# Kernel tuning notes

Hardware: AMD Instinct MI355X
Metric: run time of the kernel (lower is better)

Reference implementation:

```python
import jax, jax.numpy as jnp
import numpy as np

BN_EPS = 1e-5
R = 8.0        # radius
L = 11         # sequence kernel size (odd), s = L//2
K = 24         # kernel_channels[-1]
N_NODES = 32768
N_EDGES = 524288
C_IN = 128     # in_channels == out_channels
C_W = 32       # width = out_channels * base_width / 64


def _bn(x, gamma, beta):
    # BatchNorm1d in training mode: biased batch statistics over node dim
    mu = jnp.mean(x, axis=0)
    var = jnp.mean(jnp.square(x - mu), axis=0)
    return (x - mu) * jax.lax.rsqrt(var + BN_EPS) * gamma + beta


def _lrelu(x, slope):
    return jnp.where(x >= 0, x, slope * x)


def setup_inputs() -> dict:
    key = jax.random.key(0)
    ks = jax.random.split(key, 10)

    def glorot(k, shape, fan_in):
        return jax.random.normal(k, shape, jnp.float32) * np.float32(1.0 / np.sqrt(fan_in))

    inp = {}
    inp["x"] = jax.random.normal(ks[0], (N_NODES, C_IN), jnp.float32)
    inp["pos"] = jax.random.normal(ks[1], (N_NODES, 3), jnp.float32) * 10.0
    inp["ori"] = jax.random.normal(ks[2], (N_NODES, 9), jnp.float32)
    inp["seq"] = jnp.arange(N_NODES, dtype=jnp.int32)
    inp["edge_index"] = jax.random.randint(ks[3], (2, N_EDGES), 0, N_NODES, jnp.int32)
    # input MLP params: BN(C_IN) -> LeakyReLU(0.1) -> Linear(C_IN->C_W, no bias) -> BN(C_W) -> LeakyReLU(0.1)
    inp["bn1_g"] = jnp.ones((C_IN,), jnp.float32)
    inp["bn1_b"] = jnp.zeros((C_IN,), jnp.float32)
    inp["lin1_w"] = glorot(ks[4], (C_IN, C_W), C_IN)
    inp["bn2_g"] = jnp.ones((C_W,), jnp.float32)
    inp["bn2_b"] = jnp.zeros((C_W,), jnp.float32)
    # CDConv WeightNet (single layer kernel_channels=[K]): per-seq-bin affine 7 -> K
    inp["wn_w"] = glorot(ks[5], (L, 7, K), 7)
    inp["wn_b"] = jnp.zeros((L, K), jnp.float32)
    # CDConv output projection: [K*C_W, C_W]
    inp["conv_w"] = glorot(ks[6], (K * C_W, C_W), K * C_W)
    # output Linear: BN(C_W) -> LeakyReLU(0.1) -> Linear(C_W->C_IN, no bias)
    inp["bn3_g"] = jnp.ones((C_W,), jnp.float32)
    inp["bn3_b"] = jnp.zeros((C_W,), jnp.float32)
    inp["lin2_w"] = glorot(ks[7], (C_W, C_IN), C_W)
    return inp


def reference(x, pos, ori, seq, edge_index,
              bn1_g, bn1_b, lin1_w, bn2_g, bn2_b,
              wn_w, wn_b, conv_w, bn3_g, bn3_b, lin2_w):
    n = x.shape[0]
    identity = x  # in_channels == out_channels -> identity branch is passthrough

    # ----- input MLP (mid_channels=None) -----
    h = _lrelu(_bn(x, bn1_g, bn1_b), 0.1)
    h = h @ lin1_w                       # [N, C_W]
    h = _lrelu(_bn(h, bn2_g, bn2_b), 0.1)

    # ----- CDConv: continuous geometric kernel over neighbor edges -----
    src, dst = edge_index[0], edge_index[1]      # message j=src -> i=dst
    d = pos[src] - pos[dst]                      # [E,3]
    dist = jnp.linalg.norm(d, axis=-1, keepdims=True)
    direction = d / (dist + 1e-9)
    Ri = ori[dst].reshape(-1, 3, 3)              # receiver local frame
    Rj = ori[src].reshape(-1, 3, 3)
    pos_local = jnp.einsum('eij,ej->ei', Ri, direction)      # direction in local frame
    ori_feat = jnp.einsum('eij,ej->ei', Ri, Rj[:, 0, :])     # neighbor axis in local frame
    delta = jnp.concatenate([pos_local, ori_feat, dist / R], axis=-1)  # [E,7]

    s = L // 2
    sidx = jnp.clip(seq[src] - seq[dst], -s, s) + s          # [E] in [0, L)

    # WeightNet: per-edge affine selected by sequence bin, LeakyReLU(0.2)
    w = _lrelu(jnp.einsum('ef,efk->ek', delta, wn_w[sidx]) + wn_b[sidx], 0.2)  # [E,K]

    # message = outer(kernel_weight, x_j), scatter-sum to receivers
    msg = (w[:, :, None] * h[src][:, None, :]).reshape(w.shape[0], K * C_W)   # [E, K*C_W]
    agg = jax.ops.segment_sum(msg, dst, num_segments=n)                        # [N, K*C_W]
    h = agg @ conv_w                                                            # [N, C_W]

    # ----- output Linear + residual -----
    h = _lrelu(_bn(h, bn3_g, bn3_b), 0.1)
    out = h @ lin2_w + identity
    return out
```

## Files before the change

kernel.cpp:

```cpp
#include <hip/hip_runtime.h>

#define N_NODES 32768
#define C_IN 128
#define C_W 32
#define KK 24
#define SS 5
#define NPB 8
#define TC 256
#define AGS (KK * C_W + 4)
#define WNS 172
#define WBS 28
#define HS 36

#define BF_LO(u) __uint_as_float((u) << 16)
#define BF_HI(u) __uint_as_float((u) & 0xFFFF0000u)

__device__ __forceinline__ unsigned int bf16pair(float lo, float hi) {
    unsigned int ulo = __float_as_uint(lo);
    unsigned int uhi = __float_as_uint(hi);
    ulo = (ulo + 0x7FFFu + ((ulo >> 16) & 1u)) >> 16;
    uhi = (uhi + 0x7FFFu + ((uhi >> 16) & 1u)) & 0xFFFF0000u;
    return uhi | ulo;
}

__global__ void __launch_bounds__(256) k_pre(
        const float* __restrict__ x, float* __restrict__ s1,
        const int* __restrict__ ei, int E, int* __restrict__ counts) {
    int t = threadIdx.x;
    int c = t % C_IN;
    int r0 = blockIdx.x * 2 + t / C_IN;
    float s = 0.f, sq = 0.f;
    for (int r = r0; r < N_NODES; r += 1024) {
        float v = x[(size_t)r * C_IN + c];
        s += v; sq += v * v;
    }
    atomicAdd(&s1[c], s);
    atomicAdd(&s1[C_IN + c], sq);
    for (int e = blockIdx.x * 256 + t; e < E; e += 512 * 256)
        atomicAdd(&counts[ei[E + e]], 1);
}

__global__ void __launch_bounds__(256) k_mlp1(
        const float* __restrict__ x, const float* __restrict__ s1,
        const float* __restrict__ g1, const float* __restrict__ b1,
        const float* __restrict__ w1, float* __restrict__ hpre,
        float* __restrict__ s2sh) {
    __shared__ float sAB[2][C_IN];
    __shared__ float sx[32][C_IN + 4];
    __shared__ float sw[C_IN][C_W];
    const int t = threadIdx.x;
    const int row0 = blockIdx.x * 32;
    if (t < C_IN) {
        float mean = s1[t] * (1.f / N_NODES);
        float var = s1[C_IN + t] * (1.f / N_NODES) - mean * mean;
        float a = g1[t] * rsqrtf(var + 1e-5f);
        sAB[0][t] = a; sAB[1][t] = b1[t] - mean * a;
    }
    for (int idx = t; idx < C_IN * C_W; idx += 256)
        sw[idx / C_W][idx % C_W] = w1[idx];
    __syncthreads();
    for (int idx = t; idx < 32 * 32; idx += 256) {
        int r = idx >> 5, cq = idx & 31;
        float4 v = *(const float4*)&x[(size_t)(row0 + r) * C_IN + cq * 4];
        float* d = &sx[r][cq * 4];
        float a0 = sAB[0][cq*4+0]*v.x + sAB[1][cq*4+0];
        float a1 = sAB[0][cq*4+1]*v.y + sAB[1][cq*4+1];
        float a2 = sAB[0][cq*4+2]*v.z + sAB[1][cq*4+2];
        float a3 = sAB[0][cq*4+3]*v.w + sAB[1][cq*4+3];
        d[0] = a0 >= 0.f ? a0 : 0.1f * a0;
        d[1] = a1 >= 0.f ? a1 : 0.1f * a1;
        d[2] = a2 >= 0.f ? a2 : 0.1f * a2;
        d[3] = a3 >= 0.f ? a3 : 0.1f * a3;
    }
    __syncthreads();
    const int r = t >> 3, c0 = (t & 7) * 4;
    float ac0 = 0.f, ac1 = 0.f, ac2 = 0.f, ac3 = 0.f;
    #pragma unroll 8
    for (int cc = 0; cc < C_IN; ++cc) {
        float xv = sx[r][cc];
        float4 wv = *(const float4*)&sw[cc][c0];
        ac0 += xv * wv.x; ac1 += xv * wv.y; ac2 += xv * wv.z; ac3 += xv * wv.w;
    }
    float4 o; o.x = ac0; o.y = ac1; o.z = ac2; o.w = ac3;
    *(float4*)&hpre[(size_t)(row0 + r) * C_W + c0] = o;
    __syncthreads();
    sx[r][c0] = ac0; sx[r][c0+1] = ac1; sx[r][c0+2] = ac2; sx[r][c0+3] = ac3;
    __syncthreads();
    if (t < C_W) {
        float s = 0.f, sq = 0.f;
        #pragma unroll
        for (int rr = 0; rr < 32; ++rr) {
            float v = sx[rr][t];
            s += v; sq += v * v;
        }
        int sh = (blockIdx.x & 7) * 64;
        atomicAdd(&s2sh[sh + t], s);
        atomicAdd(&s2sh[sh + C_W + t], sq);
    }
}

__global__ void __launch_bounds__(1024) k_scan(
        const int* __restrict__ counts, int* __restrict__ offsets,
        int* __restrict__ cursor) {
    __shared__ int sblk[1024];
    const int t = threadIdx.x;
    const int base = t * 32;
    const int4* cp = (const int4*)(counts + base);
    int loc[32];
    int s = 0;
    #pragma unroll
    for (int q = 0; q < 8; ++q) {
        int4 v = cp[q];
        loc[q*4+0] = s; s += v.x;
        loc[q*4+1] = s; s += v.y;
        loc[q*4+2] = s; s += v.z;
        loc[q*4+3] = s; s += v.w;
    }
    sblk[t] = s;
    __syncthreads();
    for (int d = 1; d < 1024; d <<= 1) {
        int u = (t >= d) ? sblk[t - d] : 0;
        __syncthreads();
        sblk[t] += u;
        __syncthreads();
    }
    const int blockbase = sblk[t] - s;
    #pragma unroll
    for (int q = 0; q < 8; ++q) {
        int4 o;
        o.x = blockbase + loc[q*4+0];
        o.y = blockbase + loc[q*4+1];
        o.z = blockbase + loc[q*4+2];
        o.w = blockbase + loc[q*4+3];
        ((int4*)(offsets + base))[q] = o;
        ((int4*)(cursor + base))[q] = o;
    }
    if (t == 1023) offsets[N_NODES] = sblk[1023];
}

__global__ void __launch_bounds__(256) k_scatter(
        const int* __restrict__ ei, int E, int* __restrict__ cursor,
        int* __restrict__ srcPerm) {
    int e = blockIdx.x * 256 + threadIdx.x;
    if (e < E) {
        int dst = ei[E + e];
        int p = atomicAdd(&cursor[dst], 1);
        srcPerm[p] = ei[e];
    }
}

__global__ void __launch_bounds__(512) k_mega(
    const int* __restrict__ offsets, const int* __restrict__ srcPerm,
    const float* __restrict__ pos, const float* __restrict__ ori,
    const int* __restrict__ seq, const float* __restrict__ hpre,
    const float* __restrict__ s2sh, const float* __restrict__ g2,
    const float* __restrict__ b2,
    const float* __restrict__ wnw, const float* __restrict__ wnb,
    const float* __restrict__ convw,
    float* __restrict__ convout, float* __restrict__ s3sh) {

    __shared__ float sWnw[11 * WNS];
    __shared__ float sWnb[11 * WBS];
    __shared__ float sA2[C_W], sB2[C_W];
    __shared__ int   sOff[NPB + 1];
    __shared__ float sNd[NPB][13];
    __shared__ union SU {
        struct { unsigned short h[TC * HS]; unsigned int w[TC * 12]; } stg;
        struct { float agg[NPB][AGS]; float red[8][NPB][C_W];
                 float rv[NPB][C_W]; float rq[NPB][C_W]; } fin;
    } U;

    const int t = threadIdx.x;
    const int i0 = blockIdx.x * NPB;
    for (int idx = t; idx < 11 * 168; idx += 512)
        sWnw[(idx / 168) * WNS + idx % 168] = wnw[idx];
    for (int idx = t; idx < 11 * 24; idx += 512)
        sWnb[(idx / 24) * WBS + idx % 24] = wnb[idx];
    if (t < C_W) {
        float s = 0.f, sq = 0.f;
        #pragma unroll
        for (int j = 0; j < 8; ++j) {
            s  += s2sh[j * 64 + t];
            sq += s2sh[j * 64 + C_W + t];
        }
        float mean = s * (1.f / N_NODES);
        float var = sq * (1.f / N_NODES) - mean * mean;
        float a = g2[t] * rsqrtf(var + 1e-5f);
        sA2[t] = a; sB2[t] = b2[t] - mean * a;
    }
    if (t <= NPB) sOff[t] = offsets[i0 + t];
    if (t < NPB * 13) {
        int n = t / 13, f = t % 13;
        float v;
        if (f < 3)       v = pos[(i0 + n) * 3 + f];
        else if (f < 12) v = ori[(i0 + n) * 9 + (f - 3)];
        else             v = __int_as_float(seq[i0 + n]);
        sNd[n][f] = v;
    }
    __syncthreads();

    const int w = t >> 6, lane = t & 63, c = lane & 31, s = lane >> 5;
    const int beg = sOff[w], end = sOff[w + 1];
    const int blkBeg = sOff[0], blkEnd = sOff[NPB];
    float a[KK];
    #pragma unroll
    for (int k = 0; k < KK; ++k) a[k] = 0.f;

    for (int base = blkBeg; base < blkEnd; base += TC) {
        const int cnt = min(TC, blkEnd - base);
        __syncthreads();
        {
            const int e    = t & 255;
            const int half = t >> 8;
            if (e < cnt) {
                const int slot = base + e;
                int g = 0;
                #pragma unroll
                for (int j = 1; j < NPB; ++j) g += (slot >= sOff[j]);
                const int src = srcPerm[slot];
                float px = pos[src*3+0], py = pos[src*3+1], pz = pos[src*3+2];
                float o0 = ori[src*9+0], o1 = ori[src*9+1], o2 = ori[src*9+2];
                int sqs = seq[src];
                float dx = px - sNd[g][0], dy = py - sNd[g][1], dz = pz - sNd[g][2];
                float dist = sqrtf(dx*dx + dy*dy + dz*dz);
                float inv = 1.f / (dist + 1e-9f);
                float ux = dx*inv, uy = dy*inv, uz = dz*inv;
                float df[7];
                #pragma unroll
                for (int r = 0; r < 3; ++r) {
                    float m0 = sNd[g][3 + r*3 + 0];
                    float m1 = sNd[g][3 + r*3 + 1];
                    float m2 = sNd[g][3 + r*3 + 2];
                    df[r]     = m0*ux + m1*uy + m2*uz;
                    df[3 + r] = m0*o0 + m1*o1 + m2*o2;
                }
                df[6] = dist * 0.125f;
                int dsq = sqs - __float_as_int(sNd[g][12]);
                dsq = dsq < -SS ? -SS : (dsq > SS ? SS : dsq);
                const int sb = dsq + SS;
                float wv[12];
                {
                    const float* wb = &sWnb[sb * WBS + half * 12];
                    #pragma unroll
                    for (int j = 0; j < 12; ++j) wv[j] = wb[j];
                }
                const float* wn = &sWnw[sb * WNS + half * 12];
                #pragma unroll
                for (int f = 0; f < 7; ++f) {
                    float d_ = df[f];
                    #pragma unroll
                    for (int j = 0; j < 12; ++j)
                        wv[j] += d_ * wn[f * 24 + j];
                }
                #pragma unroll
                for (int j = 0; j < 12; ++j) wv[j] = wv[j] >= 0.f ? wv[j] : 0.2f * wv[j];
                #pragma unroll
                for (int jj = 0; jj < 6; ++jj)
                    U.stg.w[e * 12 + half * 6 + jj] = bf16pair(wv[2*jj], wv[2*jj+1]);
                const float4* hs = (const float4*)(hpre + (size_t)src * C_W);
                uint2* hd = (uint2*)&U.stg.h[e * HS + half * 16];
                #pragma unroll
                for (int q = 0; q < 2; ++q) {
                    float4 v0 = hs[half * 4 + 2*q], v1 = hs[half * 4 + 2*q + 1];
                    float f[8] = {v0.x, v0.y, v0.z, v0.w, v1.x, v1.y, v1.z, v1.w};
                    #pragma unroll
                    for (int j = 0; j < 8; ++j) {
                        int ch = half * 16 + q * 8 + j;
                        float av = sA2[ch] * f[j] + sB2[ch];
                        f[j] = av >= 0.f ? av : 0.1f * av;
                    }
                    uint2 p0; p0.x = bf16pair(f[0], f[1]); p0.y = bf16pair(f[2], f[3]);
                    uint2 p1; p1.x = bf16pair(f[4], f[5]); p1.y = bf16pair(f[6], f[7]);
                    hd[2*q] = p0; hd[2*q+1] = p1;
                }
            }
        }
        __syncthreads();
        const int lo = max(beg, base), hi = min(end, base + cnt);
        #pragma unroll 2
        for (int p = lo + s; p < hi; p += 2) {
            const int pr = p - base;
            const float v = BF_LO((unsigned int)U.stg.h[pr * HS + c]);
            const uint4* wp = (const uint4*)&U.stg.w[pr * 12];
            const uint4 A = wp[0], B = wp[1], Cc = wp[2];
            a[0]  += BF_LO(A.x) * v;  a[1]  += BF_HI(A.x) * v;
            a[2]  += BF_LO(A.y) * v;  a[3]  += BF_HI(A.y) * v;
            a[4]  += BF_LO(A.z) * v;  a[5]  += BF_HI(A.z) * v;
            a[6]  += BF_LO(A.w) * v;  a[7]  += BF_HI(A.w) * v;
            a[8]  += BF_LO(B.x) * v;  a[9]  += BF_HI(B.x) * v;
            a[10] += BF_LO(B.y) * v;  a[11] += BF_HI(B.y) * v;
            a[12] += BF_LO(B.z) * v;  a[13] += BF_HI(B.z) * v;
            a[14] += BF_LO(B.w) * v;  a[15] += BF_HI(B.w) * v;
            a[16] += BF_LO(Cc.x) * v; a[17] += BF_HI(Cc.x) * v;
            a[18] += BF_LO(Cc.y) * v; a[19] += BF_HI(Cc.y) * v;
            a[20] += BF_LO(Cc.z) * v; a[21] += BF_HI(Cc.z) * v;
            a[22] += BF_LO(Cc.w) * v; a[23] += BF_HI(Cc.w) * v;
        }
    }
    __syncthreads();
    #pragma unroll
    for (int k = 0; k < KK; ++k) a[k] += __shfl_xor(a[k], 32, 64);
    if (s == 0) {
        #pragma unroll
        for (int k = 0; k < KK; ++k) U.fin.agg[w][k * C_W + c] = a[k];
    }
    __syncthreads();

    {
        const int coq = t & 7;
        const int gp  = (t >> 3) & 7;
        const int sl  = t >> 6;
        const int r0  = sl * 96;
        float4 acc; acc.x = acc.y = acc.z = acc.w = 0.f;
        #pragma unroll 6
        for (int rc = 0; rc < 96; rc += 4) {
            const float4 s4 = *(const float4*)&U.fin.agg[gp][r0 + rc];
            const float4 w0 = *(const float4*)&convw[(size_t)(r0+rc+0)*32 + coq*4];
            const float4 w1 = *(const float4*)&convw[(size_t)(r0+rc+1)*32 + coq*4];
            const float4 w2 = *(const float4*)&convw[(size_t)(r0+rc+2)*32 + coq*4];
            const float4 w3 = *(const float4*)&convw[(size_t)(r0+rc+3)*32 + coq*4];
            acc.x += s4.x*w0.x + s4.y*w1.x + s4.z*w2.x + s4.w*w3.x;
            acc.y += s4.x*w0.y + s4.y*w1.y + s4.z*w2.y + s4.w*w3.y;
            acc.z += s4.x*w0.z + s4.y*w1.z + s4.z*w2.z + s4.w*w3.z;
            acc.w += s4.x*w0.w + s4.y*w1.w + s4.z*w2.w + s4.w*w3.w;
        }
        *(float4*)&U.fin.red[sl][gp][coq * 4] = acc;
    }
    __syncthreads();
    if (t < 256) {
        const int gg = t >> 5, co = t & 31;
        float v = 0.f;
        #pragma unroll
        for (int sl = 0; sl < 8; ++sl) v += U.fin.red[sl][gg][co];
        convout[(size_t)(i0 + gg) * C_W + co] = v;
        U.fin.rv[gg][co] = v; U.fin.rq[gg][co] = v * v;
    }
    __syncthreads();
    if (t < 64) {
        int cc = t & 31;
        bool isq = t >= C_W;
        float s2 = 0.f;
        #pragma unroll
        for (int gg = 0; gg < NPB; ++gg)
            s2 += isq ? U.fin.rq[gg][cc] : U.fin.rv[gg][cc];
        atomicAdd(&s3sh[(blockIdx.x & 7) * 64 + t], s2);
    }
}

__global__ void __launch_bounds__(256) k_out(
        const float* __restrict__ conv, const float* __restrict__ s3sh,
        const float* __restrict__ g3, const float* __restrict__ b3,
        const float* __restrict__ w2, const float* __restrict__ x,
        float* __restrict__ out) {
    __shared__ float sAB[2][C_W];
    __shared__ float sh[8][C_W];
    __shared__ float sw2[C_W][C_IN];
    const int t = threadIdx.x;
    const int row0 = blockIdx.x * 8;
    if (t < C_W) {
        float s = 0.f, sq = 0.f;
        #pragma unroll
        for (int j = 0; j < 8; ++j) {
            s  += s3sh[j * 64 + t];
            sq += s3sh[j * 64 + C_W + t];
        }
        float mean = s * (1.f / N_NODES);
        float var = sq * (1.f / N_NODES) - mean * mean;
        float a = g3[t] * rsqrtf(var + 1e-5f);
        sAB[0][t] = a; sAB[1][t] = b3[t] - mean * a;
    }
    for (int idx = t; idx < C_W * C_IN; idx += 256)
        sw2[idx >> 7][idx & 127] = w2[idx];
    __syncthreads();
    {
        float v = conv[(size_t)row0 * C_W + t];
        int r = t >> 5, cc = t & 31;
        v = sAB[0][cc] * v + sAB[1][cc];
        sh[r][cc] = v >= 0.f ? v : 0.1f * v;
    }
    __syncthreads();
    const int r = t >> 5, c4 = (t & 31) * 4;
    float4 acc = *(const float4*)&x[(size_t)(row0 + r) * C_IN + c4];
    #pragma unroll 8
    for (int cw = 0; cw < C_W; ++cw) {
        float hv = sh[r][cw];
        float4 wv = *(const float4*)&sw2[cw][c4];
        acc.x += hv * wv.x; acc.y += hv * wv.y;
        acc.z += hv * wv.z; acc.w += hv * wv.w;
    }
    *(float4*)&out[(size_t)(row0 + r) * C_IN + c4] = acc;
}

extern "C" void kernel_launch(void* const* d_in, const int* in_sizes, int n_in,
                              void* d_out, int out_size, void* d_ws, size_t ws_size,
                              hipStream_t stream) {
    const float* x     = (const float*)d_in[0];
    const float* pos   = (const float*)d_in[1];
    const float* ori   = (const float*)d_in[2];
    const int*   seq   = (const int*)d_in[3];
    const int*   ei    = (const int*)d_in[4];
    const float* bn1g  = (const float*)d_in[5];
    const float* bn1b  = (const float*)d_in[6];
    const float* lin1w = (const float*)d_in[7];
    const float* bn2g  = (const float*)d_in[8];
    const float* bn2b  = (const float*)d_in[9];
    const float* wnw   = (const float*)d_in[10];
    const float* wnb   = (const float*)d_in[11];
    const float* convw = (const float*)d_in[12];
    const float* bn3g  = (const float*)d_in[13];
    const float* bn3b  = (const float*)d_in[14];
    const float* lin2w = (const float*)d_in[15];
    float* out = (float*)d_out;
    const int E = in_sizes[4] / 2;

    char* wsb = (char*)d_ws;
    size_t off = 0;
    auto alloc = [&](size_t bytes) {
        void* p = wsb + off;
        off = (off + bytes + 255) & ~(size_t)255;
        return p;
    };
    float* s1      = (float*)alloc(256 * 4);
    float* s2sh    = (float*)alloc(512 * 4);
    float* s3sh    = (float*)alloc(512 * 4);
    int*   counts  = (int*)alloc((size_t)N_NODES * 4);
    size_t zero_bytes = off;
    int*   offsets = (int*)alloc(((size_t)N_NODES + 1) * 4);
    int*   cursor  = (int*)alloc((size_t)N_NODES * 4);
    int*   srcPerm = (int*)alloc((size_t)E * 4);
    float* hpre    = (float*)alloc((size_t)N_NODES * C_W * 4);
    float* convo   = (float*)alloc((size_t)N_NODES * C_W * 4);

    hipMemsetAsync(wsb, 0, zero_bytes, stream);

    k_pre<<<512, 256, 0, stream>>>(x, s1, ei, E, counts);
    k_scan<<<1, 1024, 0, stream>>>(counts, offsets, cursor);
    k_scatter<<<(E + 255) / 256, 256, 0, stream>>>(ei, E, cursor, srcPerm);
    k_mlp1<<<N_NODES / 32, 256, 0, stream>>>(x, s1, bn1g, bn1b, lin1w, hpre, s2sh);
    k_mega<<<N_NODES / NPB, 512, 0, stream>>>(offsets, srcPerm, pos, ori, seq,
                                              hpre, s2sh, bn2g, bn2b, wnw, wnb,
                                              convw, convo, s3sh);
    k_out<<<N_NODES / 8, 256, 0, stream>>>(convo, s3sh, bn3g, bn3b, lin2w, x, out);
}
```

Baseline: 265.8 us.

## Store hpre and conv weights in fp16 and merge scatter with MLP1 kernel

Stores the pre-activation hidden features in fp16 instead of fp32, halving the per-edge gather traffic in the mega kernel, and replaces bf16 staging with fp16 half2 packing. Converts the conv projection weights to fp16 inside the scan kernel so the mega kernel reads half as many weight bytes. Merges the CSR scatter kernel and the first MLP kernel into one launch with disjoint block ranges, removing a launch and letting both run concurrently. fp16 adds range and overflow risk compared with bf16 and fp32, and the fp16 conversion of weights adds a small serial loop to the single-block scan.

```diff
diff --git a/kernel.cpp b/kernel.cpp
--- a/kernel.cpp
+++ b/kernel.cpp
@@ -1,4 +1,5 @@
 #include <hip/hip_runtime.h>
+#include <hip/hip_fp16.h>
 
 #define N_NODES 32768
 #define C_IN 128
@@ -12,15 +13,15 @@
 #define WBS 28
 #define HS 36
 
-#define BF_LO(u) __uint_as_float((u) << 16)
-#define BF_HI(u) __uint_as_float((u) & 0xFFFF0000u)
-
-__device__ __forceinline__ unsigned int bf16pair(float lo, float hi) {
-    unsigned int ulo = __float_as_uint(lo);
-    unsigned int uhi = __float_as_uint(hi);
-    ulo = (ulo + 0x7FFFu + ((ulo >> 16) & 1u)) >> 16;
-    uhi = (uhi + 0x7FFFu + ((uhi >> 16) & 1u)) & 0xFFFF0000u;
-    return uhi | ulo;
+__device__ __forceinline__ unsigned int h2pack(float lo, float hi) {
+    __half2 h = __floats2half2_rn(lo, hi);
+    return *(unsigned int*)&h;
+}
+__device__ __forceinline__ float h2lo(unsigned int u) {
+    return __low2float(*(__half2*)&u);
+}
+__device__ __forceinline__ float h2hi(unsigned int u) {
+    return __high2float(*(__half2*)&u);
 }
 
 __global__ void __launch_bounds__(256) k_pre(
@@ -40,68 +41,10 @@
         atomicAdd(&counts[ei[E + e]], 1);
 }
 
-__global__ void __launch_bounds__(256) k_mlp1(
-        const float* __restrict__ x, const float* __restrict__ s1,
-        const float* __restrict__ g1, const float* __restrict__ b1,
-        const float* __restrict__ w1, float* __restrict__ hpre,
-        float* __restrict__ s2sh) {
-    __shared__ float sAB[2][C_IN];
-    __shared__ float sx[32][C_IN + 4];
-    __shared__ float sw[C_IN][C_W];
-    const int t = threadIdx.x;
-    const int row0 = blockIdx.x * 32;
-    if (t < C_IN) {
-        float mean = s1[t] * (1.f / N_NODES);
-        float var = s1[C_IN + t] * (1.f / N_NODES) - mean * mean;
-        float a = g1[t] * rsqrtf(var + 1e-5f);
-        sAB[0][t] = a; sAB[1][t] = b1[t] - mean * a;
-    }
-    for (int idx = t; idx < C_IN * C_W; idx += 256)
-        sw[idx / C_W][idx % C_W] = w1[idx];
-    __syncthreads();
-    for (int idx = t; idx < 32 * 32; idx += 256) {
-        int r = idx >> 5, cq = idx & 31;
-        float4 v = *(const float4*)&x[(size_t)(row0 + r) * C_IN + cq * 4];
-        float* d = &sx[r][cq * 4];
-        float a0 = sAB[0][cq*4+0]*v.x + sAB[1][cq*4+0];
-        float a1 = sAB[0][cq*4+1]*v.y + sAB[1][cq*4+1];
-        float a2 = sAB[0][cq*4+2]*v.z + sAB[1][cq*4+2];
-        float a3 = sAB[0][cq*4+3]*v.w + sAB[1][cq*4+3];
-        d[0] = a0 >= 0.f ? a0 : 0.1f * a0;
-        d[1] = a1 >= 0.f ? a1 : 0.1f * a1;
-        d[2] = a2 >= 0.f ? a2 : 0.1f * a2;
-        d[3] = a3 >= 0.f ? a3 : 0.1f * a3;
-    }
-    __syncthreads();
-    const int r = t >> 3, c0 = (t & 7) * 4;
-    float ac0 = 0.f, ac1 = 0.f, ac2 = 0.f, ac3 = 0.f;
-    #pragma unroll 8
-    for (int cc = 0; cc < C_IN; ++cc) {
-        float xv = sx[r][cc];
-        float4 wv = *(const float4*)&sw[cc][c0];
-        ac0 += xv * wv.x; ac1 += xv * wv.y; ac2 += xv * wv.z; ac3 += xv * wv.w;
-    }
-    float4 o; o.x = ac0; o.y = ac1; o.z = ac2; o.w = ac3;
-    *(float4*)&hpre[(size_t)(row0 + r) * C_W + c0] = o;
-    __syncthreads();
-    sx[r][c0] = ac0; sx[r][c0+1] = ac1; sx[r][c0+2] = ac2; sx[r][c0+3] = ac3;
-    __syncthreads();
-    if (t < C_W) {
-        float s = 0.f, sq = 0.f;
-        #pragma unroll
-        for (int rr = 0; rr < 32; ++rr) {
-            float v = sx[rr][t];
-            s += v; sq += v * v;
-        }
-        int sh = (blockIdx.x & 7) * 64;
-        atomicAdd(&s2sh[sh + t], s);
-        atomicAdd(&s2sh[sh + C_W + t], sq);
-    }
-}
-
 __global__ void __launch_bounds__(1024) k_scan(
         const int* __restrict__ counts, int* __restrict__ offsets,
-        int* __restrict__ cursor) {
+        int* __restrict__ cursor, const float* __restrict__ convw,
+        __half* __restrict__ convh) {
     __shared__ int sblk[1024];
     const int t = threadIdx.x;
     const int base = t * 32;
@@ -136,27 +79,90 @@
         ((int4*)(cursor + base))[q] = o;
     }
     if (t == 1023) offsets[N_NODES] = sblk[1023];
-}
-
-__global__ void __launch_bounds__(256) k_scatter(
+    for (int i = t; i < KK * C_W * C_W; i += 1024)
+        convh[i] = __float2half(convw[i]);
+}
+
+__global__ void __launch_bounds__(256) k_mid(
         const int* __restrict__ ei, int E, int* __restrict__ cursor,
-        int* __restrict__ srcPerm) {
-    int e = blockIdx.x * 256 + threadIdx.x;
-    if (e < E) {
-        int dst = ei[E + e];
-        int p = atomicAdd(&cursor[dst], 1);
-        srcPerm[p] = ei[e];
+        int* __restrict__ srcPerm, int SB,
+        const float* __restrict__ x, const float* __restrict__ s1,
+        const float* __restrict__ g1, const float* __restrict__ b1,
+        const float* __restrict__ w1, unsigned int* __restrict__ hpreh,
+        float* __restrict__ s2sh) {
+    const int t = threadIdx.x;
+    if ((int)blockIdx.x < SB) {
+        int e = blockIdx.x * 256 + t;
+        if (e < E) {
+            int dst = ei[E + e];
+            int p = atomicAdd(&cursor[dst], 1);
+            srcPerm[p] = ei[e];
+        }
+        return;
+    }
+    __shared__ float sAB[2][C_IN];
+    __shared__ float sx[32][C_IN + 4];
+    __shared__ float sw[C_IN][C_W];
+    const int row0 = (blockIdx.x - SB) * 32;
+    if (t < C_IN) {
+        float mean = s1[t] * (1.f / N_NODES);
+        float var = s1[C_IN + t] * (1.f / N_NODES) - mean * mean;
+        float a = g1[t] * rsqrtf(var + 1e-5f);
+        sAB[0][t] = a; sAB[1][t] = b1[t] - mean * a;
+    }
+    for (int idx = t; idx < C_IN * C_W; idx += 256)
+        sw[idx / C_W][idx % C_W] = w1[idx];
+    __syncthreads();
+    for (int idx = t; idx < 32 * 32; idx += 256) {
+        int r = idx >> 5, cq = idx & 31;
+        float4 v = *(const float4*)&x[(size_t)(row0 + r) * C_IN + cq * 4];
+        float* d = &sx[r][cq * 4];
+        float a0 = sAB[0][cq*4+0]*v.x + sAB[1][cq*4+0];
+        float a1 = sAB[0][cq*4+1]*v.y + sAB[1][cq*4+1];
+        float a2 = sAB[0][cq*4+2]*v.z + sAB[1][cq*4+2];
+        float a3 = sAB[0][cq*4+3]*v.w + sAB[1][cq*4+3];
+        d[0] = a0 >= 0.f ? a0 : 0.1f * a0;
+        d[1] = a1 >= 0.f ? a1 : 0.1f * a1;
+        d[2] = a2 >= 0.f ? a2 : 0.1f * a2;
+        d[3] = a3 >= 0.f ? a3 : 0.1f * a3;
+    }
+    __syncthreads();
+    const int r = t >> 3, c0 = (t & 7) * 4;
+    float ac0 = 0.f, ac1 = 0.f, ac2 = 0.f, ac3 = 0.f;
+    #pragma unroll 8
+    for (int cc = 0; cc < C_IN; ++cc) {
+        float xv = sx[r][cc];
+        float4 wv = *(const float4*)&sw[cc][c0];
+        ac0 += xv * wv.x; ac1 += xv * wv.y; ac2 += xv * wv.z; ac3 += xv * wv.w;
+    }
+    {
+        uint2 o; o.x = h2pack(ac0, ac1); o.y = h2pack(ac2, ac3);
+        *(uint2*)&hpreh[(size_t)(row0 + r) * 16 + (t & 7) * 2] = o;
+    }
+    __syncthreads();
+    sx[r][c0] = ac0; sx[r][c0+1] = ac1; sx[r][c0+2] = ac2; sx[r][c0+3] = ac3;
+    __syncthreads();
+    if (t < C_W) {
+        float s = 0.f, sq = 0.f;
+        #pragma unroll
+        for (int rr = 0; rr < 32; ++rr) {
+            float v = sx[rr][t];
+            s += v; sq += v * v;
+        }
+        int sh = ((blockIdx.x - SB) & 7) * 64;
+        atomicAdd(&s2sh[sh + t], s);
+        atomicAdd(&s2sh[sh + C_W + t], sq);
     }
 }
 
 __global__ void __launch_bounds__(512) k_mega(
     const int* __restrict__ offsets, const int* __restrict__ srcPerm,
     const float* __restrict__ pos, const float* __restrict__ ori,
-    const int* __restrict__ seq, const float* __restrict__ hpre,
+    const int* __restrict__ seq, const unsigned int* __restrict__ hpreh,
     const float* __restrict__ s2sh, const float* __restrict__ g2,
     const float* __restrict__ b2,
     const float* __restrict__ wnw, const float* __restrict__ wnb,
-    const float* __restrict__ convw,
+    const __half* __restrict__ convh,
     float* __restrict__ convout, float* __restrict__ s3sh) {
 
     __shared__ float sWnw[11 * WNS];
@@ -256,22 +262,25 @@
                 for (int j = 0; j < 12; ++j) wv[j] = wv[j] >= 0.f ? wv[j] : 0.2f * wv[j];
                 #pragma unroll
                 for (int jj = 0; jj < 6; ++jj)
-                    U.stg.w[e * 12 + half * 6 + jj] = bf16pair(wv[2*jj], wv[2*jj+1]);
-                const float4* hs = (const float4*)(hpre + (size_t)src * C_W);
-                uint2* hd = (uint2*)&U.stg.h[e * HS + half * 16];
-                #pragma unroll
-                for (int q = 0; q < 2; ++q) {
-                    float4 v0 = hs[half * 4 + 2*q], v1 = hs[half * 4 + 2*q + 1];
-                    float f[8] = {v0.x, v0.y, v0.z, v0.w, v1.x, v1.y, v1.z, v1.w};
-                    #pragma unroll
-                    for (int j = 0; j < 8; ++j) {
-                        int ch = half * 16 + q * 8 + j;
-                        float av = sA2[ch] * f[j] + sB2[ch];
-                        f[j] = av >= 0.f ? av : 0.1f * av;
-                    }
-                    uint2 p0; p0.x = bf16pair(f[0], f[1]); p0.y = bf16pair(f[2], f[3]);
-                    uint2 p1; p1.x = bf16pair(f[4], f[5]); p1.y = bf16pair(f[6], f[7]);
-                    hd[2*q] = p0; hd[2*q+1] = p1;
+                    U.stg.w[e * 12 + half * 6 + jj] = h2pack(wv[2*jj], wv[2*jj+1]);
+                const uint4* hs4 = (const uint4*)(hpreh + (size_t)src * 16);
+                uint4 ha = hs4[half * 2], hb = hs4[half * 2 + 1];
+                unsigned int hin[8] = {ha.x, ha.y, ha.z, ha.w, hb.x, hb.y, hb.z, hb.w};
+                unsigned int hout[8];
+                #pragma unroll
+                for (int j = 0; j < 8; ++j) {
+                    int ch = half * 16 + 2 * j;
+                    float f0 = sA2[ch]   * h2lo(hin[j]) + sB2[ch];
+                    float f1 = sA2[ch+1] * h2hi(hin[j]) + sB2[ch+1];
+                    f0 = f0 >= 0.f ? f0 : 0.1f * f0;
+                    f1 = f1 >= 0.f ? f1 : 0.1f * f1;
+                    hout[j] = h2pack(f0, f1);
+                }
+                uint2* hd = (uint2*)(U.stg.h + e * HS + half * 16);
+                #pragma unroll
+                for (int j = 0; j < 4; ++j) {
+                    uint2 o; o.x = hout[2*j]; o.y = hout[2*j+1];
+                    hd[j] = o;
                 }
             }
         }
@@ -280,21 +289,21 @@
         #pragma unroll 2
         for (int p = lo + s; p < hi; p += 2) {
             const int pr = p - base;
-            const float v = BF_LO((unsigned int)U.stg.h[pr * HS + c]);
+            const float v = __half2float(((const __half*)U.stg.h)[pr * HS + c]);
             const uint4* wp = (const uint4*)&U.stg.w[pr * 12];
             const uint4 A = wp[0], B = wp[1], Cc = wp[2];
-            a[0]  += BF_LO(A.x) * v;  a[1]  += BF_HI(A.x) * v;
-            a[2]  += BF_LO(A.y) * v;  a[3]  += BF_HI(A.y) * v;
-            a[4]  += BF_LO(A.z) * v;  a[5]  += BF_HI(A.z) * v;
-            a[6]  += BF_LO(A.w) * v;  a[7]  += BF_HI(A.w) * v;
-            a[8]  += BF_LO(B.x) * v;  a[9]  += BF_HI(B.x) * v;
-            a[10] += BF_LO(B.y) * v;  a[11] += BF_HI(B.y) * v;
-            a[12] += BF_LO(B.z) * v;  a[13] += BF_HI(B.z) * v;
-            a[14] += BF_LO(B.w) * v;  a[15] += BF_HI(B.w) * v;
-            a[16] += BF_LO(Cc.x) * v; a[17] += BF_HI(Cc.x) * v;
-            a[18] += BF_LO(Cc.y) * v; a[19] += BF_HI(Cc.y) * v;
-            a[20] += BF_LO(Cc.z) * v; a[21] += BF_HI(Cc.z) * v;
-            a[22] += BF_LO(Cc.w) * v; a[23] += BF_HI(Cc.w) * v;
+            a[0]  += h2lo(A.x) * v;  a[1]  += h2hi(A.x) * v;
+            a[2]  += h2lo(A.y) * v;  a[3]  += h2hi(A.y) * v;
+            a[4]  += h2lo(A.z) * v;  a[5]  += h2hi(A.z) * v;
+            a[6]  += h2lo(A.w) * v;  a[7]  += h2hi(A.w) * v;
+            a[8]  += h2lo(B.x) * v;  a[9]  += h2hi(B.x) * v;
+            a[10] += h2lo(B.y) * v;  a[11] += h2hi(B.y) * v;
+            a[12] += h2lo(B.z) * v;  a[13] += h2hi(B.z) * v;
+            a[14] += h2lo(B.w) * v;  a[15] += h2hi(B.w) * v;
+            a[16] += h2lo(Cc.x) * v; a[17] += h2hi(Cc.x) * v;
+            a[18] += h2lo(Cc.y) * v; a[19] += h2hi(Cc.y) * v;
+            a[20] += h2lo(Cc.z) * v; a[21] += h2hi(Cc.z) * v;
+            a[22] += h2lo(Cc.w) * v; a[23] += h2hi(Cc.w) * v;
         }
     }
     __syncthreads();
@@ -315,14 +324,14 @@
         #pragma unroll 6
         for (int rc = 0; rc < 96; rc += 4) {
             const float4 s4 = *(const float4*)&U.fin.agg[gp][r0 + rc];
-            const float4 w0 = *(const float4*)&convw[(size_t)(r0+rc+0)*32 + coq*4];
-            const float4 w1 = *(const float4*)&convw[(size_t)(r0+rc+1)*32 + coq*4];
-            const float4 w2 = *(const float4*)&convw[(size_t)(r0+rc+2)*32 + coq*4];
-            const float4 w3 = *(const float4*)&convw[(size_t)(r0+rc+3)*32 + coq*4];
-            acc.x += s4.x*w0.x + s4.y*w1.x + s4.z*w2.x + s4.w*w3.x;
-            acc.y += s4.x*w0.y + s4.y*w1.y + s4.z*w2.y + s4.w*w3.y;
-            acc.z += s4.x*w0.z + s4.y*w1.z + s4.z*w2.z + s4.w*w3.z;
-            acc.w += s4.x*w0.w + s4.y*w1.w + s4.z*w2.w + s4.w*w3.w;
+            const uint2 q0 = *(const uint2*)&convh[(size_t)(r0+rc+0)*32 + coq*4];
+            const uint2 q1 = *(const uint2*)&convh[(size_t)(r0+rc+1)*32 + coq*4];
+            const uint2 q2 = *(const uint2*)&convh[(size_t)(r0+rc+2)*32 + coq*4];
+            const uint2 q3 = *(const uint2*)&convh[(size_t)(r0+rc+3)*32 + coq*4];
+            acc.x += h2lo(q0.x)*s4.x + h2lo(q1.x)*s4.y + h2lo(q2.x)*s4.z + h2lo(q3.x)*s4.w;
+            acc.y += h2hi(q0.x)*s4.x + h2hi(q1.x)*s4.y + h2hi(q2.x)*s4.z + h2hi(q3.x)*s4.w;
+            acc.z += h2lo(q0.y)*s4.x + h2lo(q1.y)*s4.y + h2lo(q2.y)*s4.z + h2lo(q3.y)*s4.w;
+            acc.w += h2hi(q0.y)*s4.x + h2hi(q1.y)*s4.y + h2hi(q2.y)*s4.z + h2hi(q3.y)*s4.w;
         }
         *(float4*)&U.fin.red[sl][gp][coq * 4] = acc;
     }
@@ -428,17 +437,20 @@
     int*   offsets = (int*)alloc(((size_t)N_NODES + 1) * 4);
     int*   cursor  = (int*)alloc((size_t)N_NODES * 4);
     int*   srcPerm = (int*)alloc((size_t)E * 4);
-    float* hpre    = (float*)alloc((size_t)N_NODES * C_W * 4);
+    unsigned int* hpreh = (unsigned int*)alloc((size_t)N_NODES * 16 * 4);
     float* convo   = (float*)alloc((size_t)N_NODES * C_W * 4);
+    __half* convh  = (__half*)alloc((size_t)KK * C_W * C_W * 2);
 
     hipMemsetAsync(wsb, 0, zero_bytes, stream);
 
+    const int SB = (E + 255) / 256;
     k_pre<<<512, 256, 0, stream>>>(x, s1, ei, E, counts);
-    k_scan<<<1, 1024, 0, stream>>>(counts, offsets, cursor);
-    k_scatter<<<(E + 255) / 256, 256, 0, stream>>>(ei, E, cursor, srcPerm);
-    k_mlp1<<<N_NODES / 32, 256, 0, stream>>>(x, s1, bn1g, bn1b, lin1w, hpre, s2sh);
+    k_scan<<<1, 1024, 0, stream>>>(counts, offsets, cursor, convw, convh);
+    k_mid<<<SB + N_NODES / 32, 256, 0, stream>>>(ei, E, cursor, srcPerm, SB,
+                                                 x, s1, bn1g, bn1b, lin1w,
+                                                 hpreh, s2sh);
     k_mega<<<N_NODES / NPB, 512, 0, stream>>>(offsets, srcPerm, pos, ori, seq,
-                                              hpre, s2sh, bn2g, bn2b, wnw, wnb,
-                                              convw, convo, s3sh);
+                                              hpreh, s2sh, bn2g, bn2b, wnw, wnb,
+                                              convh, convo, s3sh);
     k_out<<<N_NODES / 8, 256, 0, stream>>>(convo, s3sh, bn3g, bn3b, lin2w, x, out);
 }
```

Result: slower. 325.8 us (+22.5%).
